# Kernel tuning notes

Hardware: AMD Instinct MI355X
Metric: run time of the kernel (lower is better)

The kernel has to match this reference:

```python
import jax, jax.numpy as jnp
import numpy as np

B, R, SR, K, F = 1, 2048, 24, 8, 32
DIST_FREQ = 2   # dist_xyz_freq -> PE dim 2*2*3 = 12
VIEW_FREQ = 4   # num_viewdir_freqs -> PE dim 2*4*3 = 24


def pe(x, n_freqs):
    # positional encoding: concat sin/cos of x * 2^i, flattened over last dim
    fb = (2.0 ** jnp.arange(n_freqs)).astype(x.dtype)          # [L]
    xb = x[..., None] * fb                                      # [..., 3, L]
    enc = jnp.concatenate([jnp.sin(xb), jnp.cos(xb)], axis=-1)  # [..., 3, 2L]
    return enc.reshape(*x.shape[:-1], -1)                       # [..., 3*2L]


def setup_inputs() -> dict:
    key = jax.random.key(0)
    ks = jax.random.split(key, 12)
    s = 0.1  # small init scale for weights
    return {
        'sampled_embedding': jax.random.normal(ks[0], (B, R, SR, K, F), jnp.float32),
        'dists': jax.random.normal(ks[1], (B, R, SR, K, 3), jnp.float32) * 0.1,
        'viewdirs': jax.random.normal(ks[2], (B, R, SR, 3), jnp.float32),
        'pnt_mask': jax.random.randint(ks[3], (B, R, SR, K), 0, 2, jnp.int32),
        'w1': jax.random.normal(ks[4], (F + 2 * DIST_FREQ * 3, 256), jnp.float32) * s,
        'b1': jnp.zeros((256,), jnp.float32),
        'w2': jax.random.normal(ks[5], (256, 256), jnp.float32) * s,
        'b2': jnp.zeros((256,), jnp.float32),
        'wa1': jax.random.normal(ks[6], (256, 256), jnp.float32) * s,
        'ba1': jnp.zeros((256,), jnp.float32),
        'wa2': jax.random.normal(ks[7], (256, 1), jnp.float32) * s,
        'ba2': jnp.zeros((1,), jnp.float32),
        'wc1': jax.random.normal(ks[8], (256 + 2 * VIEW_FREQ * 3, 256), jnp.float32) * s,
        'bc1': jnp.zeros((256,), jnp.float32),
        'wc2': jax.random.normal(ks[9], (256, 3), jnp.float32) * s,
        'bc2': jnp.zeros((3,), jnp.float32),
    }


def reference(sampled_embedding, dists, viewdirs, pnt_mask,
              w1, b1, w2, b2, wa1, ba1, wa2, ba2, wc1, bc1, wc2, bc2):
    mask = pnt_mask.astype(sampled_embedding.dtype)             # [B,R,SR,K]

    # quadric distance kernel -> normalized neighbor weights
    d2 = jnp.sum(dists * dists, axis=-1)                        # [B,R,SR,K]
    w = 1.0 / jnp.clip(d2, 1e-8)
    w = w * mask
    w = w / jnp.clip(jnp.sum(w, axis=-1, keepdims=True), 1e-8)  # agg_weight_norm

    # per-neighbor feature MLP (block1): feat ++ PE(dist_xyz) -> 256 -> 256
    feat_in = jnp.concatenate([sampled_embedding, pe(dists, DIST_FREQ)], axis=-1)
    h = jax.nn.relu(feat_in @ w1 + b1)
    h = jax.nn.relu(h @ w2 + b2)                                # [B,R,SR,K,256]

    # distance-weighted aggregation over neighbors (apply_pnt_mask folded into w)
    agg = jnp.einsum('brsk,brskc->brsc', w, h)                  # [B,R,SR,256]

    # alpha branch + raw2out_density (act_super: softplus(raw - 1))
    ah = jax.nn.relu(agg @ wa1 + ba1)
    density = jax.nn.softplus(ah @ wa2 + ba2 - 1.0)             # [B,R,SR,1]

    # color branch + raw2out_color (widened sigmoid)
    cin = jnp.concatenate([agg, pe(viewdirs, VIEW_FREQ)], axis=-1)
    ch = jax.nn.relu(cin @ wc1 + bc1)
    color = jax.nn.sigmoid(ch @ wc2 + bc2) * (1.0 + 2e-3) - 1e-3  # [B,R,SR,3]

    return jnp.concatenate([density, color], axis=-1)           # [B,R,SR,4]
```

## Files before the change

kernel.cpp:

```cpp
#include <hip/hip_runtime.h>

typedef unsigned short ushort_t;
typedef __bf16 bf16x8 __attribute__((ext_vector_type(8)));
typedef float f32x4 __attribute__((ext_vector_type(4)));

#define NPTS    49152
#define KNBR    8
#define PTS_A   8
#define PBLK_A  512
#define ITERS_A 12
#define PTS_B   32
#define NBLK_B  (NPTS / PTS_B)

#define W1S_OFF   0
#define W2S_OFF   16384
#define WA1S_OFF  81920
#define WC1S_OFF  147456
#define WA2S_OFF  221184
#define WC2S_OFF  225280
#define WS_WEIGHT 229376
#define AGG_OFF   229376

__device__ __forceinline__ float b2f(ushort_t u) {
    return __builtin_bit_cast(float, ((unsigned)u) << 16);
}
__device__ __forceinline__ ushort_t f2b(float f) {
    unsigned x = __builtin_bit_cast(unsigned, f);
    unsigned r = x + 0x7fffu + ((x >> 16) & 1u);
    return (ushort_t)(r >> 16);
}
__device__ __forceinline__ ushort_t f2bc(float f) {
    unsigned x = __builtin_bit_cast(unsigned, f);
    return (ushort_t)((x + 0x8000u) >> 16);
}

__global__ __launch_bounds__(256) void prep_swizzle(
    const float* __restrict__ w1, const float* __restrict__ b1,
    const float* __restrict__ w2,
    const float* __restrict__ wa1, const float* __restrict__ wc1,
    const float* __restrict__ wa2, const float* __restrict__ wc2,
    ushort_t* __restrict__ ws)
{
    int idx = blockIdx.x * 256 + threadIdx.x;
    if (idx >= WS_WEIGHT) return;

    if (idx >= WA2S_OFF) {
        int off2 = idx - WA2S_OFF;
        int mat = off2 >> 12;
        int off = off2 & 4095;
        int kb = off >> 7, rem = off & 127;
        int n = rem >> 3, j = rem & 7;
        int k = kb * 8 + j;
        float v = 0.f;
        if (mat == 0) { if (n == 0) v = wa2[k]; }
        else          { if (n < 3)  v = wc2[k * 3 + n]; }
        ws[idx] = f2b(v);
        return;
    }

    int off, base;
    if (idx < W2S_OFF) {
        off = idx; base = W1S_OFF;
        int kb = off >> 11, rem = off & 2047;
        int j = rem >> 8, n = rem & 255;
        int k = kb * 8 + j;
        float v = 0.f;
        if (k < 44)       v = w1[k * 256 + n];
        else if (k == 44) v = b1[n];
        ws[base + kb * 2048 + n * 8 + j] = f2b(v);
        return;
    }
    const float* src; int srcK;
    if (idx < WA1S_OFF)       { src = w2;  base = W2S_OFF;  off = idx - W2S_OFF;  srcK = 256; }
    else if (idx < WC1S_OFF)  { src = wa1; base = WA1S_OFF; off = idx - WA1S_OFF; srcK = 256; }
    else                      { src = wc1; base = WC1S_OFF; off = idx - WC1S_OFF; srcK = 280; }
    int kb  = off >> 11;
    int rem = off & 2047;
    int j = rem >> 8;
    int n = rem & 255;
    int k = kb * 8 + j;
    float v = (k < srcK) ? src[k * 256 + n] : 0.f;
    ws[base + kb * 2048 + n * 8 + j] = f2b(v);
}

__global__ __launch_bounds__(256, 2) void pa_mlp(
    const float* __restrict__ emb, const float* __restrict__ dists,
    const int* __restrict__ mask,  const float* __restrict__ b2,
    const ushort_t* __restrict__ ws, ushort_t* __restrict__ aggg)
{
    __shared__ __align__(16) ushort_t uH1[64 * 264];
    __shared__ __align__(16) float sWraw[64];
    __shared__ __align__(16) float sWn[64];
    ushort_t (*sFeat)[72] = (ushort_t(*)[72])uH1;
    ushort_t (*sH1)[264]  = (ushort_t(*)[264])uH1;

    const int tid  = threadIdx.x;
    const int lane = tid & 63;
    const int wv   = tid >> 6;
    const int n0   = lane & 15;
    const int quad = lane >> 4;
    const int colB = wv * 64;

    bf16x8 w2c[32];
    #pragma unroll
    for (int ki = 0; ki < 8; ki++)
        #pragma unroll
        for (int nt = 0; nt < 4; nt++)
            w2c[ki * 4 + nt] = *(const bf16x8*)(ws + W2S_OFF + ki * 8192 + quad * 2048 + (colB + nt * 16 + n0) * 8);

    #pragma unroll 1
    for (int it = 0; it < ITERS_A; it++) {
        const int blk = blockIdx.x * ITERS_A + it;
        const int pb  = blk * PTS_A;

        {
            int g0 = blk * 2048 + tid * 8;
            int r = tid >> 2, c8 = (tid & 3) * 8;
            float4 f0 = *(const float4*)(emb + g0);
            float4 f1 = *(const float4*)(emb + g0 + 4);
            ushort_t v8[8];
            v8[0] = f2bc(f0.x); v8[1] = f2bc(f0.y); v8[2] = f2bc(f0.z); v8[3] = f2bc(f0.w);
            v8[4] = f2bc(f1.x); v8[5] = f2bc(f1.y); v8[6] = f2bc(f1.z); v8[7] = f2bc(f1.w);
            *(uint4*)&sFeat[r][c8] = *(uint4*)v8;
        }
        if (tid < 64) {
            int gr = pb * KNBR + tid;
            float x = dists[gr * 3 + 0];
            float y = dists[gr * 3 + 1];
            float z = dists[gr * 3 + 2];
            float d2 = x * x + y * y + z * z;
            sWraw[tid] = (float)mask[gr] / fmaxf(d2, 1e-8f);
            float xs[3] = {x, y, z};
            #pragma unroll
            for (int d = 0; d < 3; d++) {
                #pragma unroll
                for (int l = 0; l < 2; l++) {
                    float ang = xs[d] * (float)(1 << l);
                    sFeat[tid][32 + d * 4 + l]     = f2bc(__sinf(ang));
                    sFeat[tid][32 + d * 4 + 2 + l] = f2bc(__cosf(ang));
                }
            }
            sFeat[tid][44] = 0x3F80;
            #pragma unroll
            for (int c = 45; c < 64; c++) sFeat[tid][c] = 0;
        }
        __syncthreads();
        if (tid < 64) {
            int lp = tid >> 3;
            float s = 0.f;
            #pragma unroll
            for (int k = 0; k < 8; k++) s += sWraw[lp * 8 + k];
            sWn[tid] = sWraw[tid] / fmaxf(s, 1e-8f);
        }

        f32x4 acc[16];
        #pragma unroll
        for (int i = 0; i < 16; i++) acc[i] = (f32x4){0.f, 0.f, 0.f, 0.f};

        #pragma unroll
        for (int ki = 0; ki < 2; ki++) {
            bf16x8 a[4];
            #pragma unroll
            for (int mt = 0; mt < 4; mt++)
                a[mt] = *(const bf16x8*)&sFeat[mt * 16 + n0][ki * 32 + quad * 8];
            const ushort_t* bp = ws + W1S_OFF + ki * 8192 + quad * 2048 + (colB + n0) * 8;
            #pragma unroll
            for (int nt = 0; nt < 4; nt++) {
                bf16x8 b = *(const bf16x8*)(bp + nt * 128);
                #pragma unroll
                for (int mt = 0; mt < 4; mt++)
                    acc[mt * 4 + nt] = __builtin_amdgcn_mfma_f32_16x16x32_bf16(a[mt], b, acc[mt * 4 + nt], 0, 0, 0);
            }
        }
        __syncthreads();

        {
            #pragma unroll
            for (int nt = 0; nt < 4; nt++) {
                int col = colB + nt * 16 + n0;
                #pragma unroll
                for (int mt = 0; mt < 4; mt++)
                    #pragma unroll
                    for (int r = 0; r < 4; r++)
                        sH1[mt * 16 + quad * 4 + r][col] = f2bc(fmaxf(acc[mt * 4 + nt][r], 0.f));
            }
        }
        __syncthreads();

        #pragma unroll
        for (int i = 0; i < 16; i++) acc[i] = (f32x4){0.f, 0.f, 0.f, 0.f};
        #pragma unroll
        for (int ki = 0; ki < 8; ki++) {
            bf16x8 a[4];
            #pragma unroll
            for (int mt = 0; mt < 4; mt++)
                a[mt] = *(const bf16x8*)&sH1[mt * 16 + n0][ki * 32 + quad * 8];
            #pragma unroll
            for (int nt = 0; nt < 4; nt++)
                #pragma unroll
                for (int mt = 0; mt < 4; mt++)
                    acc[mt * 4 + nt] = __builtin_amdgcn_mfma_f32_16x16x32_bf16(a[mt], w2c[ki * 4 + nt], acc[mt * 4 + nt], 0, 0, 0);
        }
        {
            #pragma unroll
            for (int mt = 0; mt < 4; mt++) {
                f32x4 wn4 = *(const f32x4*)&sWn[mt * 16 + quad * 4];
                #pragma unroll
                for (int nt = 0; nt < 4; nt++) {
                    int col = colB + nt * 16 + n0;
                    float bias = b2[col];
                    float s = fmaxf(acc[mt * 4 + nt][0] + bias, 0.f) * wn4[0]
                            + fmaxf(acc[mt * 4 + nt][1] + bias, 0.f) * wn4[1]
                            + fmaxf(acc[mt * 4 + nt][2] + bias, 0.f) * wn4[2]
                            + fmaxf(acc[mt * 4 + nt][3] + bias, 0.f) * wn4[3];
                    s += __shfl_xor(s, 16);
                    if ((quad & 1) == 0) {
                        int pt = pb + 2 * mt + (quad >> 1);
                        aggg[(size_t)pt * 256 + col] = f2bc(s);
                    }
                }
            }
        }
        __syncthreads();
    }
}

__global__ __launch_bounds__(256) void pa_branch(
    const float* __restrict__ vdirs,
    const float* __restrict__ ba1v, const float* __restrict__ ba2v,
    const float* __restrict__ bc1v, const float* __restrict__ bc2v,
    const ushort_t* __restrict__ ws, const ushort_t* __restrict__ aggg,
    float* __restrict__ out)
{
    __shared__ __align__(16) ushort_t reg1[32 * 296];
    __shared__ __align__(16) ushort_t reg2[32 * 264];
    ushort_t (*sCin)[296] = (ushort_t(*)[296])reg1;
    ushort_t (*sAh)[264]  = (ushort_t(*)[264])reg1;
    ushort_t (*sCh)[264]  = (ushort_t(*)[264])reg2;

    const int tid  = threadIdx.x;
    const int lane = tid & 63;
    const int wv   = tid >> 6;
    const int n0   = lane & 15;
    const int quad = lane >> 4;
    const int pb   = blockIdx.x * PTS_B;
    const int colB = wv * 64;

    #pragma unroll
    for (int it = 0; it < 4; it++) {
        int idx = (tid + it * 256) * 8;
        uint4 v = *(const uint4*)(aggg + (size_t)pb * 256 + idx);
        *(uint4*)&sCin[idx >> 8][idx & 255] = v;
    }
    #pragma unroll
    for (int it = 0; it < 3; it++) {
        int t = tid + it * 256;
        int p = t / 24, j = t % 24;
        int d = j >> 3, jj = j & 7, l = jj & 3, isc = jj >> 2;
        float ang = vdirs[(pb + p) * 3 + d] * (float)(1 << l);
        sCin[p][256 + j] = f2bc(isc ? __cosf(ang) : __sinf(ang));
    }
    sCin[tid >> 3][280 + (tid & 7)] = 0;
    __syncthreads();

    f32x4 accA[8], accC[8];
    #pragma unroll
    for (int i = 0; i < 8; i++) { accA[i] = (f32x4){0.f, 0.f, 0.f, 0.f}; accC[i] = accA[i]; }

    #pragma unroll
    for (int ki = 0; ki < 8; ki++) {
        bf16x8 a0 = *(const bf16x8*)&sCin[n0][ki * 32 + quad * 8];
        bf16x8 a1 = *(const bf16x8*)&sCin[16 + n0][ki * 32 + quad * 8];
        const ushort_t* bp = ws + WA1S_OFF + ki * 8192 + quad * 2048 + (colB + n0) * 8;
        #pragma unroll
        for (int nt = 0; nt < 4; nt++) {
            bf16x8 b = *(const bf16x8*)(bp + nt * 128);
            accA[nt]     = __builtin_amdgcn_mfma_f32_16x16x32_bf16(a0, b, accA[nt], 0, 0, 0);
            accA[4 + nt] = __builtin_amdgcn_mfma_f32_16x16x32_bf16(a1, b, accA[4 + nt], 0, 0, 0);
        }
    }
    #pragma unroll
    for (int ki = 0; ki < 9; ki++) {
        bf16x8 a0 = *(const bf16x8*)&sCin[n0][ki * 32 + quad * 8];
        bf16x8 a1 = *(const bf16x8*)&sCin[16 + n0][ki * 32 + quad * 8];
        const ushort_t* bp = ws + WC1S_OFF + ki * 8192 + quad * 2048 + (colB + n0) * 8;
        #pragma unroll
        for (int nt = 0; nt < 4; nt++) {
            bf16x8 b = *(const bf16x8*)(bp + nt * 128);
            accC[nt]     = __builtin_amdgcn_mfma_f32_16x16x32_bf16(a0, b, accC[nt], 0, 0, 0);
            accC[4 + nt] = __builtin_amdgcn_mfma_f32_16x16x32_bf16(a1, b, accC[4 + nt], 0, 0, 0);
        }
    }
    __syncthreads();

    #pragma unroll
    for (int nt = 0; nt < 4; nt++) {
        int col = colB + nt * 16 + n0;
        float biasA = ba1v[col];
        float biasC = bc1v[col];
        #pragma unroll
        for (int mt = 0; mt < 2; mt++)
            #pragma unroll
            for (int r = 0; r < 4; r++) {
                int row = mt * 16 + quad * 4 + r;
                sAh[row][col] = f2bc(fmaxf(accA[mt * 4 + nt][r] + biasA, 0.f));
                sCh[row][col] = f2bc(fmaxf(accC[mt * 4 + nt][r] + biasC, 0.f));
            }
    }
    __syncthreads();

    {
        const int isColor = wv >> 1;
        const int baseM   = (wv & 1) * 16;
        const ushort_t* A = isColor ? &sCh[0][0] : &sAh[0][0];
        const ushort_t* B = ws + (isColor ? WC2S_OFF : WA2S_OFF);
        f32x4 acc4 = (f32x4){0.f, 0.f, 0.f, 0.f};
        #pragma unroll
        for (int ki = 0; ki < 8; ki++) {
            bf16x8 a = *(const bf16x8*)(A + (baseM + n0) * 264 + ki * 32 + quad * 8);
            bf16x8 b = *(const bf16x8*)(B + ki * 512 + quad * 128 + n0 * 8);
            acc4 = __builtin_amdgcn_mfma_f32_16x16x32_bf16(a, b, acc4, 0, 0, 0);
        }
        if (!isColor) {
            if (n0 == 0) {
                float ba2s = ba2v[0];
                #pragma unroll
                for (int r = 0; r < 4; r++) {
                    int gp = pb + baseM + quad * 4 + r;
                    float yv = acc4[r] + ba2s - 1.0f;
                    out[(size_t)gp * 4] = (yv > 20.f) ? yv : log1pf(expf(yv));
                }
            }
        } else {
            if (n0 < 3) {
                float bc2s = bc2v[n0];
                #pragma unroll
                for (int r = 0; r < 4; r++) {
                    int gp = pb + baseM + quad * 4 + r;
                    float sig = 1.f / (1.f + expf(-(acc4[r] + bc2s)));
                    out[(size_t)gp * 4 + 1 + n0] = sig * (1.0f + 2e-3f) - 1e-3f;
                }
            }
        }
    }
}

extern "C" void kernel_launch(void* const* d_in, const int* in_sizes, int n_in,
                              void* d_out, int out_size, void* d_ws, size_t ws_size,
                              hipStream_t stream) {
    const float* emb   = (const float*)d_in[0];
    const float* dists = (const float*)d_in[1];
    const float* vdir  = (const float*)d_in[2];
    const int*   mask  = (const int*)d_in[3];
    const float* w1    = (const float*)d_in[4];
    const float* b1    = (const float*)d_in[5];
    const float* w2    = (const float*)d_in[6];
    const float* b2    = (const float*)d_in[7];
    const float* wa1   = (const float*)d_in[8];
    const float* ba1   = (const float*)d_in[9];
    const float* wa2   = (const float*)d_in[10];
    const float* ba2   = (const float*)d_in[11];
    const float* wc1   = (const float*)d_in[12];
    const float* bc1   = (const float*)d_in[13];
    const float* wc2   = (const float*)d_in[14];
    const float* bc2   = (const float*)d_in[15];
    ushort_t* ws  = (ushort_t*)d_ws;
    float*    out = (float*)d_out;

    prep_swizzle<<<dim3((WS_WEIGHT + 255) / 256), dim3(256), 0, stream>>>(
        w1, b1, w2, wa1, wc1, wa2, wc2, ws);
    pa_mlp<<<dim3(PBLK_A), dim3(256), 0, stream>>>(
        emb, dists, mask, b2, ws, ws + AGG_OFF);
    pa_branch<<<dim3(NBLK_B), dim3(256), 0, stream>>>(
        vdir, ba1, ba2, bc1, bc2, ws, ws + AGG_OFF, out);
}
```

Before: 224.8 us.

## Drop persistent register-cached W2 loop and split branch kernel across 512 threads

The per-neighbor MLP kernel stops being persistent: instead of 512 blocks each looping over 12 tiles with W2 fragments held in 32 vector registers, it launches one block per 8-point tile and streams W2 fragments from global/L2 inside the inner loop. This frees registers and removes the launch-bounds occupancy hint, at the cost of re-reading W2 from cache for every tile. The branch kernel now uses 512 threads so alpha and color first-layer GEMMs run on separate wave groups in parallel rather than sequentially in the same waves. The output-layer MFMAs now run on half of those waves.

```diff
diff --git a/kernel.cpp b/kernel.cpp
--- a/kernel.cpp
+++ b/kernel.cpp
@@ -7,8 +7,7 @@
 #define NPTS    49152
 #define KNBR    8
 #define PTS_A   8
-#define PBLK_A  512
-#define ITERS_A 12
+#define NBLK_A  (NPTS / PTS_A)
 #define PTS_B   32
 #define NBLK_B  (NPTS / PTS_B)
 
@@ -58,19 +57,17 @@
         return;
     }
 
-    int off, base;
     if (idx < W2S_OFF) {
-        off = idx; base = W1S_OFF;
-        int kb = off >> 11, rem = off & 2047;
+        int kb = idx >> 11, rem = idx & 2047;
         int j = rem >> 8, n = rem & 255;
         int k = kb * 8 + j;
         float v = 0.f;
         if (k < 44)       v = w1[k * 256 + n];
         else if (k == 44) v = b1[n];
-        ws[base + kb * 2048 + n * 8 + j] = f2b(v);
+        ws[W1S_OFF + kb * 2048 + n * 8 + j] = f2b(v);
         return;
     }
-    const float* src; int srcK;
+    const float* src; int off, srcK, base;
     if (idx < WA1S_OFF)       { src = w2;  base = W2S_OFF;  off = idx - W2S_OFF;  srcK = 256; }
     else if (idx < WC1S_OFF)  { src = wa1; base = WA1S_OFF; off = idx - WA1S_OFF; srcK = 256; }
     else                      { src = wc1; base = WC1S_OFF; off = idx - WC1S_OFF; srcK = 280; }
@@ -83,7 +80,7 @@
     ws[base + kb * 2048 + n * 8 + j] = f2b(v);
 }
 
-__global__ __launch_bounds__(256, 2) void pa_mlp(
+__global__ __launch_bounds__(256) void pa_mlp(
     const float* __restrict__ emb, const float* __restrict__ dists,
     const int* __restrict__ mask,  const float* __restrict__ b2,
     const ushort_t* __restrict__ ws, ushort_t* __restrict__ aggg)
@@ -99,133 +96,123 @@
     const int wv   = tid >> 6;
     const int n0   = lane & 15;
     const int quad = lane >> 4;
+    const int pb   = blockIdx.x * PTS_A;
     const int colB = wv * 64;
 
-    bf16x8 w2c[32];
-    #pragma unroll
-    for (int ki = 0; ki < 8; ki++)
-        #pragma unroll
-        for (int nt = 0; nt < 4; nt++)
-            w2c[ki * 4 + nt] = *(const bf16x8*)(ws + W2S_OFF + ki * 8192 + quad * 2048 + (colB + nt * 16 + n0) * 8);
-
-    #pragma unroll 1
-    for (int it = 0; it < ITERS_A; it++) {
-        const int blk = blockIdx.x * ITERS_A + it;
-        const int pb  = blk * PTS_A;
-
-        {
-            int g0 = blk * 2048 + tid * 8;
-            int r = tid >> 2, c8 = (tid & 3) * 8;
-            float4 f0 = *(const float4*)(emb + g0);
-            float4 f1 = *(const float4*)(emb + g0 + 4);
-            ushort_t v8[8];
-            v8[0] = f2bc(f0.x); v8[1] = f2bc(f0.y); v8[2] = f2bc(f0.z); v8[3] = f2bc(f0.w);
-            v8[4] = f2bc(f1.x); v8[5] = f2bc(f1.y); v8[6] = f2bc(f1.z); v8[7] = f2bc(f1.w);
-            *(uint4*)&sFeat[r][c8] = *(uint4*)v8;
-        }
-        if (tid < 64) {
-            int gr = pb * KNBR + tid;
-            float x = dists[gr * 3 + 0];
-            float y = dists[gr * 3 + 1];
-            float z = dists[gr * 3 + 2];
-            float d2 = x * x + y * y + z * z;
-            sWraw[tid] = (float)mask[gr] / fmaxf(d2, 1e-8f);
-            float xs[3] = {x, y, z};
-            #pragma unroll
-            for (int d = 0; d < 3; d++) {
+    {
+        int g0 = blockIdx.x * 2048 + tid * 8;
+        int r = tid >> 2, c8 = (tid & 3) * 8;
+        float4 f0 = *(const float4*)(emb + g0);
+        float4 f1 = *(const float4*)(emb + g0 + 4);
+        ushort_t v8[8];
+        v8[0] = f2bc(f0.x); v8[1] = f2bc(f0.y); v8[2] = f2bc(f0.z); v8[3] = f2bc(f0.w);
+        v8[4] = f2bc(f1.x); v8[5] = f2bc(f1.y); v8[6] = f2bc(f1.z); v8[7] = f2bc(f1.w);
+        *(uint4*)&sFeat[r][c8] = *(uint4*)v8;
+    }
+    if (tid < 64) {
+        int gr = pb * KNBR + tid;
+        float x = dists[gr * 3 + 0];
+        float y = dists[gr * 3 + 1];
+        float z = dists[gr * 3 + 2];
+        float d2 = x * x + y * y + z * z;
+        sWraw[tid] = (float)mask[gr] / fmaxf(d2, 1e-8f);
+        float xs[3] = {x, y, z};
+        #pragma unroll
+        for (int d = 0; d < 3; d++) {
+            #pragma unroll
+            for (int l = 0; l < 2; l++) {
+                float ang = xs[d] * (float)(1 << l);
+                sFeat[tid][32 + d * 4 + l]     = f2bc(__sinf(ang));
+                sFeat[tid][32 + d * 4 + 2 + l] = f2bc(__cosf(ang));
+            }
+        }
+        sFeat[tid][44] = 0x3F80;
+        #pragma unroll
+        for (int c = 45; c < 64; c++) sFeat[tid][c] = 0;
+    }
+    __syncthreads();
+    if (tid < 64) {
+        int lp = tid >> 3;
+        float s = 0.f;
+        #pragma unroll
+        for (int k = 0; k < 8; k++) s += sWraw[lp * 8 + k];
+        sWn[tid] = sWraw[tid] / fmaxf(s, 1e-8f);
+    }
+
+    f32x4 acc[16];
+    #pragma unroll
+    for (int i = 0; i < 16; i++) acc[i] = (f32x4){0.f, 0.f, 0.f, 0.f};
+
+    #pragma unroll
+    for (int ki = 0; ki < 2; ki++) {
+        bf16x8 a[4];
+        #pragma unroll
+        for (int mt = 0; mt < 4; mt++)
+            a[mt] = *(const bf16x8*)&sFeat[mt * 16 + n0][ki * 32 + quad * 8];
+        const ushort_t* bp = ws + W1S_OFF + ki * 8192 + quad * 2048 + (colB + n0) * 8;
+        #pragma unroll
+        for (int nt = 0; nt < 4; nt++) {
+            bf16x8 b = *(const bf16x8*)(bp + nt * 128);
+            #pragma unroll
+            for (int mt = 0; mt < 4; mt++)
+                acc[mt * 4 + nt] = __builtin_amdgcn_mfma_f32_16x16x32_bf16(a[mt], b, acc[mt * 4 + nt], 0, 0, 0);
+        }
+    }
+    __syncthreads();
+
+    {
+        #pragma unroll
+        for (int nt = 0; nt < 4; nt++) {
+            int col = colB + nt * 16 + n0;
+            #pragma unroll
+            for (int mt = 0; mt < 4; mt++)
                 #pragma unroll
-                for (int l = 0; l < 2; l++) {
-                    float ang = xs[d] * (float)(1 << l);
-                    sFeat[tid][32 + d * 4 + l]     = f2bc(__sinf(ang));
-                    sFeat[tid][32 + d * 4 + 2 + l] = f2bc(__cosf(ang));
+                for (int r = 0; r < 4; r++)
+                    sH1[mt * 16 + quad * 4 + r][col] = f2bc(fmaxf(acc[mt * 4 + nt][r], 0.f));
+        }
+    }
+    __syncthreads();
+
+    #pragma unroll
+    for (int i = 0; i < 16; i++) acc[i] = (f32x4){0.f, 0.f, 0.f, 0.f};
+    #pragma unroll
+    for (int ki = 0; ki < 8; ki++) {
+        bf16x8 a[4];
+        #pragma unroll
+        for (int mt = 0; mt < 4; mt++)
+            a[mt] = *(const bf16x8*)&sH1[mt * 16 + n0][ki * 32 + quad * 8];
+        const ushort_t* bp = ws + W2S_OFF + ki * 8192 + quad * 2048 + (colB + n0) * 8;
+        #pragma unroll
+        for (int nt = 0; nt < 4; nt++) {
+            bf16x8 b = *(const bf16x8*)(bp + nt * 128);
+            #pragma unroll
+            for (int mt = 0; mt < 4; mt++)
+                acc[mt * 4 + nt] = __builtin_amdgcn_mfma_f32_16x16x32_bf16(a[mt], b, acc[mt * 4 + nt], 0, 0, 0);
+        }
+    }
+    {
+        #pragma unroll
+        for (int mt = 0; mt < 4; mt++) {
+            f32x4 wn4 = *(const f32x4*)&sWn[mt * 16 + quad * 4];
+            #pragma unroll
+            for (int nt = 0; nt < 4; nt++) {
+                int col = colB + nt * 16 + n0;
+                float bias = b2[col];
+                float s = fmaxf(acc[mt * 4 + nt][0] + bias, 0.f) * wn4[0]
+                        + fmaxf(acc[mt * 4 + nt][1] + bias, 0.f) * wn4[1]
+                        + fmaxf(acc[mt * 4 + nt][2] + bias, 0.f) * wn4[2]
+                        + fmaxf(acc[mt * 4 + nt][3] + bias, 0.f) * wn4[3];
+                s += __shfl_xor(s, 16);
+                if ((quad & 1) == 0) {
+                    int pt = pb + 2 * mt + (quad >> 1);
+                    aggg[(size_t)pt * 256 + col] = f2bc(s);
                 }
             }
-            sFeat[tid][44] = 0x3F80;
-            #pragma unroll
-            for (int c = 45; c < 64; c++) sFeat[tid][c] = 0;
-        }
-        __syncthreads();
-        if (tid < 64) {
-            int lp = tid >> 3;
-            float s = 0.f;
-            #pragma unroll
-            for (int k = 0; k < 8; k++) s += sWraw[lp * 8 + k];
-            sWn[tid] = sWraw[tid] / fmaxf(s, 1e-8f);
-        }
-
-        f32x4 acc[16];
-        #pragma unroll
-        for (int i = 0; i < 16; i++) acc[i] = (f32x4){0.f, 0.f, 0.f, 0.f};
-
-        #pragma unroll
-        for (int ki = 0; ki < 2; ki++) {
-            bf16x8 a[4];
-            #pragma unroll
-            for (int mt = 0; mt < 4; mt++)
-                a[mt] = *(const bf16x8*)&sFeat[mt * 16 + n0][ki * 32 + quad * 8];
-            const ushort_t* bp = ws + W1S_OFF + ki * 8192 + quad * 2048 + (colB + n0) * 8;
-            #pragma unroll
-            for (int nt = 0; nt < 4; nt++) {
-                bf16x8 b = *(const bf16x8*)(bp + nt * 128);
-                #pragma unroll
-                for (int mt = 0; mt < 4; mt++)
-                    acc[mt * 4 + nt] = __builtin_amdgcn_mfma_f32_16x16x32_bf16(a[mt], b, acc[mt * 4 + nt], 0, 0, 0);
-            }
-        }
-        __syncthreads();
-
-        {
-            #pragma unroll
-            for (int nt = 0; nt < 4; nt++) {
-                int col = colB + nt * 16 + n0;
-                #pragma unroll
-                for (int mt = 0; mt < 4; mt++)
-                    #pragma unroll
-                    for (int r = 0; r < 4; r++)
-                        sH1[mt * 16 + quad * 4 + r][col] = f2bc(fmaxf(acc[mt * 4 + nt][r], 0.f));
-            }
-        }
-        __syncthreads();
-
-        #pragma unroll
-        for (int i = 0; i < 16; i++) acc[i] = (f32x4){0.f, 0.f, 0.f, 0.f};
-        #pragma unroll
-        for (int ki = 0; ki < 8; ki++) {
-            bf16x8 a[4];
-            #pragma unroll
-            for (int mt = 0; mt < 4; mt++)
-                a[mt] = *(const bf16x8*)&sH1[mt * 16 + n0][ki * 32 + quad * 8];
-            #pragma unroll
-            for (int nt = 0; nt < 4; nt++)
-                #pragma unroll
-                for (int mt = 0; mt < 4; mt++)
-                    acc[mt * 4 + nt] = __builtin_amdgcn_mfma_f32_16x16x32_bf16(a[mt], w2c[ki * 4 + nt], acc[mt * 4 + nt], 0, 0, 0);
-        }
-        {
-            #pragma unroll
-            for (int mt = 0; mt < 4; mt++) {
-                f32x4 wn4 = *(const f32x4*)&sWn[mt * 16 + quad * 4];
-                #pragma unroll
-                for (int nt = 0; nt < 4; nt++) {
-                    int col = colB + nt * 16 + n0;
-                    float bias = b2[col];
-                    float s = fmaxf(acc[mt * 4 + nt][0] + bias, 0.f) * wn4[0]
-                            + fmaxf(acc[mt * 4 + nt][1] + bias, 0.f) * wn4[1]
-                            + fmaxf(acc[mt * 4 + nt][2] + bias, 0.f) * wn4[2]
-                            + fmaxf(acc[mt * 4 + nt][3] + bias, 0.f) * wn4[3];
-                    s += __shfl_xor(s, 16);
-                    if ((quad & 1) == 0) {
-                        int pt = pb + 2 * mt + (quad >> 1);
-                        aggg[(size_t)pt * 256 + col] = f2bc(s);
-                    }
-                }
-            }
-        }
-        __syncthreads();
-    }
-}
-
-__global__ __launch_bounds__(256) void pa_branch(
+        }
+    }
+}
+
+__global__ __launch_bounds__(512) void pa_branch(
     const float* __restrict__ vdirs,
     const float* __restrict__ ba1v, const float* __restrict__ ba2v,
     const float* __restrict__ bc1v, const float* __restrict__ bc2v,
@@ -241,83 +228,86 @@
     const int tid  = threadIdx.x;
     const int lane = tid & 63;
     const int wv   = tid >> 6;
+    const int sub  = wv & 3;
+    const int isColor = wv >> 2;
     const int n0   = lane & 15;
     const int quad = lane >> 4;
     const int pb   = blockIdx.x * PTS_B;
-    const int colB = wv * 64;
-
-    #pragma unroll
-    for (int it = 0; it < 4; it++) {
-        int idx = (tid + it * 256) * 8;
+    const int colB = sub * 64;
+
+    #pragma unroll
+    for (int it = 0; it < 2; it++) {
+        int idx = (tid + it * 512) * 8;
         uint4 v = *(const uint4*)(aggg + (size_t)pb * 256 + idx);
         *(uint4*)&sCin[idx >> 8][idx & 255] = v;
     }
     #pragma unroll
-    for (int it = 0; it < 3; it++) {
-        int t = tid + it * 256;
-        int p = t / 24, j = t % 24;
-        int d = j >> 3, jj = j & 7, l = jj & 3, isc = jj >> 2;
-        float ang = vdirs[(pb + p) * 3 + d] * (float)(1 << l);
-        sCin[p][256 + j] = f2bc(isc ? __cosf(ang) : __sinf(ang));
-    }
-    sCin[tid >> 3][280 + (tid & 7)] = 0;
-    __syncthreads();
-
-    f32x4 accA[8], accC[8];
-    #pragma unroll
-    for (int i = 0; i < 8; i++) { accA[i] = (f32x4){0.f, 0.f, 0.f, 0.f}; accC[i] = accA[i]; }
-
+    for (int it = 0; it < 2; it++) {
+        int t = tid + it * 512;
+        if (t < 768) {
+            int p = t / 24, j = t % 24;
+            int d = j >> 3, jj = j & 7, l = jj & 3, isc = jj >> 2;
+            float ang = vdirs[(pb + p) * 3 + d] * (float)(1 << l);
+            sCin[p][256 + j] = f2bc(isc ? __cosf(ang) : __sinf(ang));
+        }
+    }
+    if (tid < 256) sCin[tid >> 3][280 + (tid & 7)] = 0;
+    __syncthreads();
+
+    f32x4 acc[8];
+    #pragma unroll
+    for (int i = 0; i < 8; i++) acc[i] = (f32x4){0.f, 0.f, 0.f, 0.f};
+    const int wOff = isColor ? WC1S_OFF : WA1S_OFF;
     #pragma unroll
     for (int ki = 0; ki < 8; ki++) {
         bf16x8 a0 = *(const bf16x8*)&sCin[n0][ki * 32 + quad * 8];
         bf16x8 a1 = *(const bf16x8*)&sCin[16 + n0][ki * 32 + quad * 8];
-        const ushort_t* bp = ws + WA1S_OFF + ki * 8192 + quad * 2048 + (colB + n0) * 8;
+        const ushort_t* bp = ws + wOff + ki * 8192 + quad * 2048 + (colB + n0) * 8;
         #pragma unroll
         for (int nt = 0; nt < 4; nt++) {
             bf16x8 b = *(const bf16x8*)(bp + nt * 128);
-            accA[nt]     = __builtin_amdgcn_mfma_f32_16x16x32_bf16(a0, b, accA[nt], 0, 0, 0);
-            accA[4 + nt] = __builtin_amdgcn_mfma_f32_16x16x32_bf16(a1, b, accA[4 + nt], 0, 0, 0);
-        }
-    }
-    #pragma unroll
-    for (int ki = 0; ki < 9; ki++) {
-        bf16x8 a0 = *(const bf16x8*)&sCin[n0][ki * 32 + quad * 8];
-        bf16x8 a1 = *(const bf16x8*)&sCin[16 + n0][ki * 32 + quad * 8];
-        const ushort_t* bp = ws + WC1S_OFF + ki * 8192 + quad * 2048 + (colB + n0) * 8;
+            acc[nt]     = __builtin_amdgcn_mfma_f32_16x16x32_bf16(a0, b, acc[nt], 0, 0, 0);
+            acc[4 + nt] = __builtin_amdgcn_mfma_f32_16x16x32_bf16(a1, b, acc[4 + nt], 0, 0, 0);
+        }
+    }
+    if (isColor) {
+        bf16x8 a0 = *(const bf16x8*)&sCin[n0][256 + quad * 8];
+        bf16x8 a1 = *(const bf16x8*)&sCin[16 + n0][256 + quad * 8];
+        const ushort_t* bp = ws + WC1S_OFF + 8 * 8192 + quad * 2048 + (colB + n0) * 8;
         #pragma unroll
         for (int nt = 0; nt < 4; nt++) {
             bf16x8 b = *(const bf16x8*)(bp + nt * 128);
-            accC[nt]     = __builtin_amdgcn_mfma_f32_16x16x32_bf16(a0, b, accC[nt], 0, 0, 0);
-            accC[4 + nt] = __builtin_amdgcn_mfma_f32_16x16x32_bf16(a1, b, accC[4 + nt], 0, 0, 0);
-        }
-    }
-    __syncthreads();
-
-    #pragma unroll
-    for (int nt = 0; nt < 4; nt++) {
-        int col = colB + nt * 16 + n0;
-        float biasA = ba1v[col];
-        float biasC = bc1v[col];
-        #pragma unroll
-        for (int mt = 0; mt < 2; mt++)
-            #pragma unroll
-            for (int r = 0; r < 4; r++) {
-                int row = mt * 16 + quad * 4 + r;
-                sAh[row][col] = f2bc(fmaxf(accA[mt * 4 + nt][r] + biasA, 0.f));
-                sCh[row][col] = f2bc(fmaxf(accC[mt * 4 + nt][r] + biasC, 0.f));
-            }
+            acc[nt]     = __builtin_amdgcn_mfma_f32_16x16x32_bf16(a0, b, acc[nt], 0, 0, 0);
+            acc[4 + nt] = __builtin_amdgcn_mfma_f32_16x16x32_bf16(a1, b, acc[4 + nt], 0, 0, 0);
+        }
     }
     __syncthreads();
 
     {
-        const int isColor = wv >> 1;
-        const int baseM   = (wv & 1) * 16;
+        const float* bv = isColor ? bc1v : ba1v;
+        ushort_t* dst = isColor ? &sCh[0][0] : &sAh[0][0];
+        #pragma unroll
+        for (int nt = 0; nt < 4; nt++) {
+            int col = colB + nt * 16 + n0;
+            float bias = bv[col];
+            #pragma unroll
+            for (int mt = 0; mt < 2; mt++)
+                #pragma unroll
+                for (int r = 0; r < 4; r++) {
+                    int row = mt * 16 + quad * 4 + r;
+                    dst[row * 264 + col] = f2bc(fmaxf(acc[mt * 4 + nt][r] + bias, 0.f));
+                }
+        }
+    }
+    __syncthreads();
+
+    if (sub < 2) {
         const ushort_t* A = isColor ? &sCh[0][0] : &sAh[0][0];
         const ushort_t* B = ws + (isColor ? WC2S_OFF : WA2S_OFF);
         f32x4 acc4 = (f32x4){0.f, 0.f, 0.f, 0.f};
         #pragma unroll
         for (int ki = 0; ki < 8; ki++) {
-            bf16x8 a = *(const bf16x8*)(A + (baseM + n0) * 264 + ki * 32 + quad * 8);
+            bf16x8 a = *(const bf16x8*)(A + (sub * 16 + n0) * 264 + ki * 32 + quad * 8);
             bf16x8 b = *(const bf16x8*)(B + ki * 512 + quad * 128 + n0 * 8);
             acc4 = __builtin_amdgcn_mfma_f32_16x16x32_bf16(a, b, acc4, 0, 0, 0);
         }
@@ -326,7 +316,7 @@
                 float ba2s = ba2v[0];
                 #pragma unroll
                 for (int r = 0; r < 4; r++) {
-                    int gp = pb + baseM + quad * 4 + r;
+                    int gp = pb + sub * 16 + quad * 4 + r;
                     float yv = acc4[r] + ba2s - 1.0f;
                     out[(size_t)gp * 4] = (yv > 20.f) ? yv : log1pf(expf(yv));
                 }
@@ -336,7 +326,7 @@
                 float bc2s = bc2v[n0];
                 #pragma unroll
                 for (int r = 0; r < 4; r++) {
-                    int gp = pb + baseM + quad * 4 + r;
+                    int gp = pb + sub * 16 + quad * 4 + r;
                     float sig = 1.f / (1.f + expf(-(acc4[r] + bc2s)));
                     out[(size_t)gp * 4 + 1 + n0] = sig * (1.0f + 2e-3f) - 1e-3f;
                 }
@@ -369,8 +359,8 @@
 
     prep_swizzle<<<dim3((WS_WEIGHT + 255) / 256), dim3(256), 0, stream>>>(
         w1, b1, w2, wa1, wc1, wa2, wc2, ws);
-    pa_mlp<<<dim3(PBLK_A), dim3(256), 0, stream>>>(
+    pa_mlp<<<dim3(NBLK_A), dim3(256), 0, stream>>>(
         emb, dists, mask, b2, ws, ws + AGG_OFF);
-    pa_branch<<<dim3(NBLK_B), dim3(256), 0, stream>>>(
+    pa_branch<<<dim3(NBLK_B), dim3(512), 0, stream>>>(
         vdir, ba1, ba2, bc1, bc2, ws, ws + AGG_OFF, out);
 }
```

Measured after the change: 223.0 us. Within noise of the previous version (-0.8%).
